# Optimization experiments

Hardware: AMD Instinct MI355X
Metric: run time of the kernel (lower is better)

The kernel has to match this reference:

```python
import jax, jax.numpy as jnp
import numpy as np

N_EMBED = 1024
N_HEAD = 16
BLOCK_SIZE = 2048
ROPE_BASE = 10000.0


def _rope_cache():
    # theta uses n_embed (full model dim) as denominator, as in the source,
    # then is truncated to head_size//2 frequencies.
    hs_half = N_EMBED // N_HEAD // 2
    j = jnp.arange(N_EMBED // 2, dtype=jnp.float32)
    theta = jnp.power(ROPE_BASE, -2.0 * j / N_EMBED)
    seq_idx = jnp.arange(BLOCK_SIZE, dtype=jnp.float32)
    idx_theta = jnp.einsum('i,j->ij', seq_idx, theta)[:, :hs_half]  # [block, hs/2]
    return jnp.stack([jnp.cos(idx_theta), jnp.sin(idx_theta)], axis=-1)  # [block, hs/2, 2]


def _apply_rope(x, cache):
    # x: [B, nh, T, hs]. FAITHFUL to source: rope indexes its cache by dim-1,
    # which here is the HEAD dim (rope is called after transpose(1,2)).
    B, d1, d2, hs = x.shape
    rc = cache[:d1, :hs // 2]            # [d1, hs/2, 2]
    rc = rc[None, :, None, :, :]          # [1, d1, 1, hs/2, 2]
    x2 = x.reshape(B, d1, d2, hs // 2, 2)
    cos, sin = rc[..., 0], rc[..., 1]
    xr, xi = x2[..., 0], x2[..., 1]
    rot = jnp.stack([xr * cos - xi * sin, xi * cos + xr * sin], axis=-1)
    return rot.reshape(B, d1, d2, hs).astype(x.dtype)


def setup_inputs() -> dict:
    key = jax.random.key(0)
    ks = jax.random.split(key, 5)
    B, T, C = 2, 2048, N_EMBED
    return {
        'x': jax.random.normal(ks[0], (B, T, C), dtype=jnp.float32),
        'w_attn': jax.random.normal(ks[1], (C, 3 * C), dtype=jnp.float32) * 0.02,
        'b_attn': jax.random.normal(ks[2], (3 * C,), dtype=jnp.float32) * 0.02,
        'w_proj': jax.random.normal(ks[3], (C, C), dtype=jnp.float32) * 0.02,
        'b_proj': jax.random.normal(ks[4], (C,), dtype=jnp.float32) * 0.02,
    }


def reference(x, w_attn, b_attn, w_proj, b_proj):
    B, T, C = x.shape
    nh, hs = N_HEAD, C // N_HEAD
    qkv = x @ w_attn + b_attn                     # [B, T, 3C]
    q, k, v = jnp.split(qkv, 3, axis=-1)
    q = q.reshape(B, T, nh, hs).transpose(0, 2, 1, 3)  # [B, nh, T, hs]
    k = k.reshape(B, T, nh, hs).transpose(0, 2, 1, 3)
    v = v.reshape(B, T, nh, hs).transpose(0, 2, 1, 3)
    cache = _rope_cache()
    q = _apply_rope(q, cache)
    k = _apply_rope(k, cache)
    scale = 1.0 / jnp.sqrt(jnp.asarray(hs, dtype=q.dtype))
    scores = jnp.einsum('bhqd,bhkd->bhqk', q, k) * scale
    causal = jnp.tril(jnp.ones((T, T), dtype=bool))
    scores = jnp.where(causal[None, None], scores, jnp.finfo(scores.dtype).min)
    attn = jax.nn.softmax(scores, axis=-1)
    y = jnp.einsum('bhqk,bhkd->bhqd', attn, v)    # [B, nh, T, hs]
    y = y.transpose(0, 2, 1, 3).reshape(B, T, C)
    return y @ w_proj + b_proj
```

## Files before the change

kernel.cpp:

```cpp
#include <hip/hip_runtime.h>
#include <hip/hip_bf16.h>
#include <math.h>

#define TSEQ 2048
#define CEMB 1024
#define NHEAD 16
#define HS 64

typedef __attribute__((ext_vector_type(8))) short bf16x8;
typedef __attribute__((ext_vector_type(4))) float f32x4;
typedef __attribute__((ext_vector_type(16))) float f32x16;
typedef unsigned int u32;

__device__ __forceinline__ void gload16(const void* g, void* l) {
    __builtin_amdgcn_global_load_lds(
        (const __attribute__((address_space(1))) unsigned int*)g,
        (__attribute__((address_space(3))) unsigned int*)l, 16, 0, 0);
}

__device__ __forceinline__ u32 pk2(float a, float b) {
    union { u32 u; __hip_bfloat16 h[2]; } t;
    t.h[0] = __float2bfloat16(a); t.h[1] = __float2bfloat16(b);
    return t.u;
}

__global__ void rope_tbl_k(float* __restrict__ tbl) {
    int i = blockIdx.x * blockDim.x + threadIdx.x;
    if (i >= NHEAD * 32) return;
    int h = i >> 5, j = i & 31;
    double theta = pow(10000.0, -2.0 * (double)j / 1024.0);
    double ang = (double)h * theta;
    tbl[2 * i + 0] = (float)cos(ang);
    tbl[2 * i + 1] = (float)sin(ang);
}

__global__ __launch_bounds__(256) void cvt_bf16_k(const float* __restrict__ in,
                                                  __hip_bfloat16* __restrict__ out) {
    int i = (blockIdx.x * 256 + threadIdx.x) * 8;
    float4 a = *(const float4*)(in + i);
    float4 b = *(const float4*)(in + i + 4);
    union { bf16x8 v; __hip_bfloat16 h[8]; } pk;
    pk.h[0] = __float2bfloat16(a.x); pk.h[1] = __float2bfloat16(a.y);
    pk.h[2] = __float2bfloat16(a.z); pk.h[3] = __float2bfloat16(a.w);
    pk.h[4] = __float2bfloat16(b.x); pk.h[5] = __float2bfloat16(b.y);
    pk.h[6] = __float2bfloat16(b.z); pk.h[7] = __float2bfloat16(b.w);
    *(bf16x8*)(out + i) = pk.v;
}

__global__ __launch_bounds__(256) void transpose_bf16_k(const float* __restrict__ src,
                                                        __hip_bfloat16* __restrict__ dst,
                                                        int K, int N) {
    __shared__ float tile[32][33];
    int n0 = blockIdx.x * 32, k0 = blockIdx.y * 32;
    int tx = threadIdx.x & 31, ty = threadIdx.x >> 5;
#pragma unroll
    for (int i = 0; i < 32; i += 8)
        tile[ty + i][tx] = src[(size_t)(k0 + ty + i) * N + n0 + tx];
    __syncthreads();
#pragma unroll
    for (int i = 0; i < 32; i += 8)
        dst[(size_t)(n0 + ty + i) * K + k0 + tx] = __float2bfloat16(tile[tx][ty + i]);
}

__global__ __launch_bounds__(256) void qkv_mfma_k(
    const __hip_bfloat16* __restrict__ Xb, const __hip_bfloat16* __restrict__ Wt,
    const float* __restrict__ bias, const float* __restrict__ tbl,
    __hip_bfloat16* __restrict__ Qb, __hip_bfloat16* __restrict__ Kb,
    __hip_bfloat16* __restrict__ Vtb)
{
    __shared__ __hip_bfloat16 Al[2][128 * 32];
    __shared__ __hip_bfloat16 Bl[2][128 * 32];
    const int tid = threadIdx.x;
    const int lane = tid & 63, w = tid >> 6;
    const int lr = lane & 15, lg = lane >> 4;
    const int wm = w >> 1, wn = w & 1;
    const int n0 = blockIdx.x * 128;
    const int m0 = blockIdx.y * 128;
    const __hip_bfloat16* gA = Xb + (size_t)(m0 + (tid >> 2)) * CEMB + (tid & 3) * 8;
    const __hip_bfloat16* gB = Wt + (size_t)(n0 + (tid >> 2)) * CEMB + (tid & 3) * 8;
#define QSTAGE(buf, kk) do { \
        gload16(gA + (kk), &Al[buf][tid * 8]); \
        gload16(gA + 64 * CEMB + (kk), &Al[buf][2048 + tid * 8]); \
        gload16(gB + (kk), &Bl[buf][tid * 8]); \
        gload16(gB + 64 * CEMB + (kk), &Bl[buf][2048 + tid * 8]); } while (0)
    f32x4 acc[4][4] = {};
    QSTAGE(0, 0);
    __syncthreads();
    for (int k0 = 0; k0 < CEMB; k0 += 32) {
        const int cur = (k0 >> 5) & 1;
        if (k0 + 32 < CEMB) QSTAGE(cur ^ 1, k0 + 32);
        bf16x8 af[4], bfr[4];
#pragma unroll
        for (int mi = 0; mi < 4; ++mi)
            af[mi] = *(const bf16x8*)&Al[cur][(wm * 64 + mi * 16 + lr) * 32 + lg * 8];
#pragma unroll
        for (int ni = 0; ni < 4; ++ni)
            bfr[ni] = *(const bf16x8*)&Bl[cur][(wn * 64 + ni * 16 + lr) * 32 + lg * 8];
#pragma unroll
        for (int mi = 0; mi < 4; ++mi)
#pragma unroll
            for (int ni = 0; ni < 4; ++ni)
                acc[mi][ni] = __builtin_amdgcn_mfma_f32_16x16x32_bf16(af[mi], bfr[ni], acc[mi][ni], 0, 0, 0);
        __syncthreads();
    }
    const int sec = (n0 >> 10);
#pragma unroll
    for (int mi = 0; mi < 4; ++mi) {
#pragma unroll
        for (int ni = 0; ni < 4; ++ni) {
            const int gcol = n0 + wn * 64 + ni * 16 + lr;
            const int c63 = gcol & 63;
            const int h = (gcol & 1023) >> 6;
            const int j = c63 >> 1;
            const float cth = tbl[(h * 32 + j) * 2 + 0];
            const float sth = tbl[(h * 32 + j) * 2 + 1];
            const float bv = bias[gcol];
            const int growb = m0 + wm * 64 + mi * 16 + lg * 4;
            const int bb = growb >> 11;
            const int t0 = growb & 2047;
            if (sec == 2) {
                union { unsigned long long u; __hip_bfloat16 hh[4]; } pk;
#pragma unroll
                for (int r = 0; r < 4; ++r) pk.hh[r] = __float2bfloat16(acc[mi][ni][r] + bv);
                *(unsigned long long*)&Vtb[(((size_t)bb * NHEAD + h) * HS + c63) * TSEQ + t0] = pk.u;
            } else {
                const float sc = (sec == 0) ? 0.18033688011112042f : 1.0f;
                __hip_bfloat16* dst = (sec == 0) ? Qb : Kb;
#pragma unroll
                for (int r = 0; r < 4; ++r) {
                    float val = acc[mi][ni][r] + bv;
                    float prt = __shfl_xor(val, 1);
                    float rot = (lr & 1) ? (val * cth + prt * sth) : (val * cth - prt * sth);
                    dst[(((size_t)bb * NHEAD + h) * TSEQ + t0 + r) * HS + c63] = __float2bfloat16(rot * sc);
                }
            }
        }
    }
#undef QSTAGE
}

__global__ __launch_bounds__(128) void attn_k(
    const __hip_bfloat16* __restrict__ Q, const __hip_bfloat16* __restrict__ K,
    const __hip_bfloat16* __restrict__ Vt, __hip_bfloat16* __restrict__ Y)
{
    __shared__ __hip_bfloat16 KsBuf[2][64 * 64];
    __shared__ __hip_bfloat16 VsBuf[2][64 * 64];
    const int tid = threadIdx.x;
    const int w = tid >> 6;
    const int lane = tid & 63;
    const int l31 = lane & 31;
    const int hi = lane >> 5;
    const int id = blockIdx.x;
    const int bh = id & 31;
    const int qb = id >> 5;
    const size_t bho = (size_t)bh * TSEQ * HS;
    const int qw = qb * 64 + w * 32;

    int srcK[4], srcV[4];
#pragma unroll
    for (int j = 0; j < 4; ++j) {
        int L = (tid + 128 * j) * 16;
        int row = L >> 7;
        int ce = ((L & 127) ^ (((row ^ (row >> 3)) & 7) << 4)) >> 1;
        srcK[j] = row * HS + ce;
        srcV[j] = row * TSEQ + ce;
    }
    const __hip_bfloat16* Kg = K + bho;
    const __hip_bfloat16* Vg = Vt + bho;
#define ASTAGE(buf, kt_) do { \
        const __hip_bfloat16* kg_ = Kg + (size_t)(kt_) * 64 * HS; \
        const __hip_bfloat16* vg_ = Vg + (size_t)(kt_) * 64; \
        char* kb_ = (char*)KsBuf[buf]; char* vb_ = (char*)VsBuf[buf]; \
        _Pragma("unroll") \
        for (int j = 0; j < 4; ++j) { \
            gload16(kg_ + srcK[j], kb_ + (tid + 128 * j) * 16); \
            gload16(vg_ + srcV[j], vb_ + (tid + 128 * j) * 16); } } while (0)

    bf16x8 qf[4];
    {
        const __hip_bfloat16* qp = Q + bho + (size_t)(qw + l31) * HS + hi * 8;
#pragma unroll
        for (int kb = 0; kb < 4; ++kb) qf[kb] = *(const bf16x8*)(qp + kb * 16);
    }
    const int base0 = l31 * 128;
    const int swz0 = ((l31 ^ (l31 >> 3)) & 7) << 4;
    const int r32 = 32 + l31;
    const int base1 = r32 * 128;
    const int swz1 = ((r32 ^ (r32 >> 3)) & 7) << 4;

    float mrow = -1e30f, lsum = 0.f;
    f32x16 o0 = {}, o1 = {};

    ASTAGE(0, 0);
    __syncthreads();
    for (int kt = 0; kt <= qb; ++kt) {
        const int cur = kt & 1;
        if (kt < qb) ASTAGE(cur ^ 1, kt + 1);
        const char* KsB = (const char*)KsBuf[cur];
        const char* VsB = (const char*)VsBuf[cur];
        const bool do1 = (w == 1) || (kt < qb);
        f32x16 s0 = {}, s1 = {};
#pragma unroll
        for (int kb = 0; kb < 4; ++kb) {
            bf16x8 kf = *(const bf16x8*)(KsB + base0 + ((kb * 32 + hi * 16) ^ swz0));
            s0 = __builtin_amdgcn_mfma_f32_32x32x16_bf16(kf, qf[kb], s0, 0, 0, 0);
        }
        if (do1) {
#pragma unroll
            for (int kb = 0; kb < 4; ++kb) {
                bf16x8 kf = *(const bf16x8*)(KsB + base1 + ((kb * 32 + hi * 16) ^ swz1));
                s1 = __builtin_amdgcn_mfma_f32_32x32x16_bf16(kf, qf[kb], s1, 0, 0, 0);
            }
        }
        if (kt == qb) {
            if (w == 0) {
#pragma unroll
                for (int r = 0; r < 16; ++r) {
                    int crow = (r & 3) + 8 * (r >> 2) + 4 * hi;
                    if (crow > l31) s0[r] = -1e30f;
                }
            } else {
#pragma unroll
                for (int r = 0; r < 16; ++r) {
                    int crow = (r & 3) + 8 * (r >> 2) + 4 * hi;
                    if (crow > l31) s1[r] = -1e30f;
                }
            }
        }
        float mx = s0[0];
#pragma unroll
        for (int r = 1; r < 16; ++r) mx = fmaxf(mx, s0[r]);
        if (do1) {
#pragma unroll
            for (int r = 0; r < 16; ++r) mx = fmaxf(mx, s1[r]);
        }
        mx = fmaxf(mx, __shfl_xor(mx, 32));
        const float mn = fmaxf(mrow, mx);
        const float alpha = __builtin_amdgcn_exp2f(mrow - mn);
        mrow = mn;
        float ls = 0.f;
#pragma unroll
        for (int r = 0; r < 16; ++r) { s0[r] = __builtin_amdgcn_exp2f(s0[r] - mn); ls += s0[r]; }
        if (do1) {
#pragma unroll
            for (int r = 0; r < 16; ++r) { s1[r] = __builtin_amdgcn_exp2f(s1[r] - mn); ls += s1[r]; }
        }
        ls += __shfl_xor(ls, 32);
        lsum = lsum * alpha + ls;
        o0 = o0 * alpha;
        o1 = o1 * alpha;
        union { u32 u[4]; bf16x8 v; } pa[4];
        {
            u32 w01 = pk2(s0[0], s0[1]),   w23 = pk2(s0[2], s0[3]);
            u32 w45 = pk2(s0[4], s0[5]),   w67 = pk2(s0[6], s0[7]);
            u32 w89 = pk2(s0[8], s0[9]),   wab = pk2(s0[10], s0[11]);
            u32 wcd = pk2(s0[12], s0[13]), wef = pk2(s0[14], s0[15]);
            u32 xa = __shfl_xor(hi ? w01 : w45, 32);
            u32 xb = __shfl_xor(hi ? w23 : w67, 32);
            u32 xc = __shfl_xor(hi ? w89 : wcd, 32);
            u32 xd = __shfl_xor(hi ? wab : wef, 32);
            if (hi == 0) {
                pa[0].u[0] = w01; pa[0].u[1] = w23; pa[0].u[2] = xa;  pa[0].u[3] = xb;
                pa[1].u[0] = w89; pa[1].u[1] = wab; pa[1].u[2] = xc;  pa[1].u[3] = xd;
            } else {
                pa[0].u[0] = xa;  pa[0].u[1] = xb;  pa[0].u[2] = w45; pa[0].u[3] = w67;
                pa[1].u[0] = xc;  pa[1].u[1] = xd;  pa[1].u[2] = wcd; pa[1].u[3] = wef;
            }
        }
        if (do1) {
            u32 w01 = pk2(s1[0], s1[1]),   w23 = pk2(s1[2], s1[3]);
            u32 w45 = pk2(s1[4], s1[5]),   w67 = pk2(s1[6], s1[7]);
            u32 w89 = pk2(s1[8], s1[9]),   wab = pk2(s1[10], s1[11]);
            u32 wcd = pk2(s1[12], s1[13]), wef = pk2(s1[14], s1[15]);
            u32 xa = __shfl_xor(hi ? w01 : w45, 32);
            u32 xb = __shfl_xor(hi ? w23 : w67, 32);
            u32 xc = __shfl_xor(hi ? w89 : wcd, 32);
            u32 xd = __shfl_xor(hi ? wab : wef, 32);
            if (hi == 0) {
                pa[2].u[0] = w01; pa[2].u[1] = w23; pa[2].u[2] = xa;  pa[2].u[3] = xb;
                pa[3].u[0] = w89; pa[3].u[1] = wab; pa[3].u[2] = xc;  pa[3].u[3] = xd;
            } else {
                pa[2].u[0] = xa;  pa[2].u[1] = xb;  pa[2].u[2] = w45; pa[2].u[3] = w67;
                pa[3].u[0] = xc;  pa[3].u[1] = xd;  pa[3].u[2] = wcd; pa[3].u[3] = wef;
            }
        }
#pragma unroll
        for (int ks = 0; ks < 2; ++ks) {
            bf16x8 vf0 = *(const bf16x8*)(VsB + base0 + ((ks * 32 + hi * 16) ^ swz0));
            o0 = __builtin_amdgcn_mfma_f32_32x32x16_bf16(vf0, pa[ks].v, o0, 0, 0, 0);
            bf16x8 vf1 = *(const bf16x8*)(VsB + base1 + ((ks * 32 + hi * 16) ^ swz1));
            o1 = __builtin_amdgcn_mfma_f32_32x32x16_bf16(vf1, pa[ks].v, o1, 0, 0, 0);
        }
        if (do1) {
#pragma unroll
            for (int ks = 2; ks < 4; ++ks) {
                bf16x8 vf0 = *(const bf16x8*)(VsB + base0 + ((ks * 32 + hi * 16) ^ swz0));
                o0 = __builtin_amdgcn_mfma_f32_32x32x16_bf16(vf0, pa[ks].v, o0, 0, 0, 0);
                bf16x8 vf1 = *(const bf16x8*)(VsB + base1 + ((ks * 32 + hi * 16) ^ swz1));
                o1 = __builtin_amdgcn_mfma_f32_32x32x16_bf16(vf1, pa[ks].v, o1, 0, 0, 0);
            }
        }
        __syncthreads();
    }
    __syncthreads();
    {
        char* T = (char*)KsBuf[0] + w * 4096;
        const float inv = 1.f / lsum;
        const int tsw = (l31 & 7) << 4;
#pragma unroll
        for (int r = 0; r < 16; ++r) {
            int d0 = (r & 3) + 8 * (r >> 2) + 4 * hi;
            *(__hip_bfloat16*)(T + base0 + ((d0 * 2) ^ tsw)) = __float2bfloat16(o0[r] * inv);
            *(__hip_bfloat16*)(T + base0 + (((d0 + 32) * 2) ^ tsw)) = __float2bfloat16(o1[r] * inv);
        }
        const int b = bh >> 4, h = bh & 15;
#pragma unroll
        for (int p = 0; p < 4; ++p) {
            int q = p * 8 + (lane >> 3);
            int colb = ((lane & 7) * 16) ^ ((q & 7) << 4);
            bf16x8 v = *(const bf16x8*)(T + q * 128 + colb);
            *(bf16x8*)(Y + ((size_t)b * TSEQ + qw + q) * CEMB + h * HS + (lane & 7) * 8) = v;
        }
    }
#undef ASTAGE
}

__global__ __launch_bounds__(256) void proj_mfma_k(
    const __hip_bfloat16* __restrict__ Ab, const __hip_bfloat16* __restrict__ Wt,
    const float* __restrict__ bias, float* __restrict__ out)
{
    __shared__ __hip_bfloat16 Al[2][128 * 32];
    __shared__ __hip_bfloat16 Bl[2][128 * 32];
    const int tid = threadIdx.x;
    const int lane = tid & 63, w = tid >> 6;
    const int lr = lane & 15, lg = lane >> 4;
    const int wm = w >> 1, wn = w & 1;
    const int n0 = blockIdx.x * 128;
    const int m0 = blockIdx.y * 128;
    const __hip_bfloat16* gA = Ab + (size_t)(m0 + (tid >> 2)) * CEMB + (tid & 3) * 8;
    const __hip_bfloat16* gB = Wt + (size_t)(n0 + (tid >> 2)) * CEMB + (tid & 3) * 8;
#define PSTAGE(buf, kk) do { \
        gload16(gA + (kk), &Al[buf][tid * 8]); \
        gload16(gA + 64 * CEMB + (kk), &Al[buf][2048 + tid * 8]); \
        gload16(gB + (kk), &Bl[buf][tid * 8]); \
        gload16(gB + 64 * CEMB + (kk), &Bl[buf][2048 + tid * 8]); } while (0)
    f32x4 acc[4][4] = {};
    PSTAGE(0, 0);
    __syncthreads();
    for (int k0 = 0; k0 < CEMB; k0 += 32) {
        const int cur = (k0 >> 5) & 1;
        if (k0 + 32 < CEMB) PSTAGE(cur ^ 1, k0 + 32);
        bf16x8 af[4], bfr[4];
#pragma unroll
        for (int mi = 0; mi < 4; ++mi)
            af[mi] = *(const bf16x8*)&Al[cur][(wm * 64 + mi * 16 + lr) * 32 + lg * 8];
#pragma unroll
        for (int ni = 0; ni < 4; ++ni)
            bfr[ni] = *(const bf16x8*)&Bl[cur][(wn * 64 + ni * 16 + lr) * 32 + lg * 8];
#pragma unroll
        for (int mi = 0; mi < 4; ++mi)
#pragma unroll
            for (int ni = 0; ni < 4; ++ni)
                acc[mi][ni] = __builtin_amdgcn_mfma_f32_16x16x32_bf16(af[mi], bfr[ni], acc[mi][ni], 0, 0, 0);
        __syncthreads();
    }
#pragma unroll
    for (int mi = 0; mi < 4; ++mi) {
#pragma unroll
        for (int ni = 0; ni < 4; ++ni) {
            const int gcol = n0 + wn * 64 + ni * 16 + lr;
            const float bv = bias[gcol];
            const int growb = m0 + wm * 64 + mi * 16 + lg * 4;
#pragma unroll
            for (int r = 0; r < 4; ++r)
                out[(size_t)(growb + r) * CEMB + gcol] = acc[mi][ni][r] + bv;
        }
    }
#undef PSTAGE
}

extern "C" void kernel_launch(void* const* d_in, const int* in_sizes, int n_in,
                              void* d_out, int out_size, void* d_ws, size_t ws_size,
                              hipStream_t stream)
{
    const float* x      = (const float*)d_in[0];
    const float* w_attn = (const float*)d_in[1];
    const float* b_attn = (const float*)d_in[2];
    const float* w_proj = (const float*)d_in[3];
    const float* b_proj = (const float*)d_in[4];
    float* out = (float*)d_out;
    char* base = (char*)d_ws;

    const size_t MB = 1048576;
    float* tbl          = (float*)base;
    __hip_bfloat16* Xb  = (__hip_bfloat16*)(base + 4096);
    __hip_bfloat16* Wta = (__hip_bfloat16*)(base + 4096 + 8 * MB);
    __hip_bfloat16* Wpt = (__hip_bfloat16*)(base + 4096 + 14 * MB);
    __hip_bfloat16* Qb  = (__hip_bfloat16*)(base + 4096 + 16 * MB);
    __hip_bfloat16* Kb  = (__hip_bfloat16*)(base + 4096 + 24 * MB);
    __hip_bfloat16* Vtb = (__hip_bfloat16*)(base + 4096 + 32 * MB);
    __hip_bfloat16* Yb  = Xb;

    rope_tbl_k<<<1, 512, 0, stream>>>(tbl);
    cvt_bf16_k<<<2048, 256, 0, stream>>>(x, Xb);
    transpose_bf16_k<<<dim3(96, 32), 256, 0, stream>>>(w_attn, Wta, CEMB, 3 * CEMB);
    transpose_bf16_k<<<dim3(32, 32), 256, 0, stream>>>(w_proj, Wpt, CEMB, CEMB);
    qkv_mfma_k<<<dim3(24, 32), 256, 0, stream>>>(Xb, Wta, b_attn, tbl, Qb, Kb, Vtb);
    attn_k<<<1024, 128, 0, stream>>>(Qb, Kb, Vtb, Yb);
    proj_mfma_k<<<dim3(8, 32), 256, 0, stream>>>(Yb, Wpt, b_proj, out);
}
```

Measured before the change: 149.7 us.

## Stage V-transpose stores through LDS, serpentine q-block order, MFMA priority hints

The QKV GEMM epilogue for the V section now writes the tile into a swizzled LDS buffer, then each thread emits 16-byte contiguous stores to the transposed V layout instead of scattered 8-byte stores. The attention kernel remaps block IDs so q-blocks are visited in a serpentine order within groups of eight, which spreads causal work more evenly across concurrently running blocks. It also raises wave priority around the MFMA sections with s_setprio. Costs are an extra LDS round trip and barrier in the V epilogue, plus scheduling behaviour that may depend on occupancy.

```diff
diff --git a/kernel.cpp b/kernel.cpp
--- a/kernel.cpp
+++ b/kernel.cpp
@@ -11,6 +11,7 @@
 typedef __attribute__((ext_vector_type(4))) float f32x4;
 typedef __attribute__((ext_vector_type(16))) float f32x16;
 typedef unsigned int u32;
+typedef unsigned long long u64;
 
 __device__ __forceinline__ void gload16(const void* g, void* l) {
     __builtin_amdgcn_global_load_lds(
@@ -68,8 +69,7 @@
     __hip_bfloat16* __restrict__ Qb, __hip_bfloat16* __restrict__ Kb,
     __hip_bfloat16* __restrict__ Vtb)
 {
-    __shared__ __hip_bfloat16 Al[2][128 * 32];
-    __shared__ __hip_bfloat16 Bl[2][128 * 32];
+    __shared__ __hip_bfloat16 SM[4][128 * 32];
     const int tid = threadIdx.x;
     const int lane = tid & 63, w = tid >> 6;
     const int lr = lane & 15, lg = lane >> 4;
@@ -79,10 +79,10 @@
     const __hip_bfloat16* gA = Xb + (size_t)(m0 + (tid >> 2)) * CEMB + (tid & 3) * 8;
     const __hip_bfloat16* gB = Wt + (size_t)(n0 + (tid >> 2)) * CEMB + (tid & 3) * 8;
 #define QSTAGE(buf, kk) do { \
-        gload16(gA + (kk), &Al[buf][tid * 8]); \
-        gload16(gA + 64 * CEMB + (kk), &Al[buf][2048 + tid * 8]); \
-        gload16(gB + (kk), &Bl[buf][tid * 8]); \
-        gload16(gB + 64 * CEMB + (kk), &Bl[buf][2048 + tid * 8]); } while (0)
+        gload16(gA + (kk), &SM[buf][tid * 8]); \
+        gload16(gA + 64 * CEMB + (kk), &SM[buf][2048 + tid * 8]); \
+        gload16(gB + (kk), &SM[2 + (buf)][tid * 8]); \
+        gload16(gB + 64 * CEMB + (kk), &SM[2 + (buf)][2048 + tid * 8]); } while (0)
     f32x4 acc[4][4] = {};
     QSTAGE(0, 0);
     __syncthreads();
@@ -92,10 +92,10 @@
         bf16x8 af[4], bfr[4];
 #pragma unroll
         for (int mi = 0; mi < 4; ++mi)
-            af[mi] = *(const bf16x8*)&Al[cur][(wm * 64 + mi * 16 + lr) * 32 + lg * 8];
+            af[mi] = *(const bf16x8*)&SM[cur][(wm * 64 + mi * 16 + lr) * 32 + lg * 8];
 #pragma unroll
         for (int ni = 0; ni < 4; ++ni)
-            bfr[ni] = *(const bf16x8*)&Bl[cur][(wn * 64 + ni * 16 + lr) * 32 + lg * 8];
+            bfr[ni] = *(const bf16x8*)&SM[2 + cur][(wn * 64 + ni * 16 + lr) * 32 + lg * 8];
 #pragma unroll
         for (int mi = 0; mi < 4; ++mi)
 #pragma unroll
@@ -104,26 +104,46 @@
         __syncthreads();
     }
     const int sec = (n0 >> 10);
-#pragma unroll
-    for (int mi = 0; mi < 4; ++mi) {
-#pragma unroll
-        for (int ni = 0; ni < 4; ++ni) {
-            const int gcol = n0 + wn * 64 + ni * 16 + lr;
-            const int c63 = gcol & 63;
-            const int h = (gcol & 1023) >> 6;
-            const int j = c63 >> 1;
-            const float cth = tbl[(h * 32 + j) * 2 + 0];
-            const float sth = tbl[(h * 32 + j) * 2 + 1];
-            const float bv = bias[gcol];
-            const int growb = m0 + wm * 64 + mi * 16 + lg * 4;
-            const int bb = growb >> 11;
-            const int t0 = growb & 2047;
-            if (sec == 2) {
-                union { unsigned long long u; __hip_bfloat16 hh[4]; } pk;
+    const int bb = m0 >> 11;
+    const int t0v = m0 & 2047;
+    if (sec == 2) {
+        char* T = (char*)SM;
+#pragma unroll
+        for (int mi = 0; mi < 4; ++mi) {
+#pragma unroll
+            for (int ni = 0; ni < 4; ++ni) {
+                const int nl = wn * 64 + ni * 16 + lr;
+                const float bv = bias[n0 + nl];
+                const int mb = wm * 64 + mi * 16 + lg * 4;
+                union { u64 u; __hip_bfloat16 hh[4]; } pk;
 #pragma unroll
                 for (int r = 0; r < 4; ++r) pk.hh[r] = __float2bfloat16(acc[mi][ni][r] + bv);
-                *(unsigned long long*)&Vtb[(((size_t)bb * NHEAD + h) * HS + c63) * TSEQ + t0] = pk.u;
-            } else {
+                *(u64*)(T + nl * 256 + ((mb * 2) ^ ((nl & 7) << 4))) = pk.u;
+            }
+        }
+        __syncthreads();
+        const int h0 = (n0 & 1023) >> 6;
+#pragma unroll
+        for (int i = 0; i < 8; ++i) {
+            int cid = tid + 256 * i;
+            int n = cid >> 4, mc = cid & 15;
+            bf16x8 v = *(const bf16x8*)(T + n * 256 + ((mc * 16) ^ ((n & 7) << 4)));
+            *(bf16x8*)&Vtb[(((size_t)bb * NHEAD + h0 + (n >> 6)) * HS + (n & 63)) * TSEQ + t0v + mc * 8] = v;
+        }
+    } else {
+#pragma unroll
+        for (int mi = 0; mi < 4; ++mi) {
+#pragma unroll
+            for (int ni = 0; ni < 4; ++ni) {
+                const int gcol = n0 + wn * 64 + ni * 16 + lr;
+                const int c63 = gcol & 63;
+                const int h = (gcol & 1023) >> 6;
+                const int j = c63 >> 1;
+                const float cth = tbl[(h * 32 + j) * 2 + 0];
+                const float sth = tbl[(h * 32 + j) * 2 + 1];
+                const float bv = bias[gcol];
+                const int growb = m0 + wm * 64 + mi * 16 + lg * 4;
+                const int t0 = growb & 2047;
                 const float sc = (sec == 0) ? 0.18033688011112042f : 1.0f;
                 __hip_bfloat16* dst = (sec == 0) ? Qb : Kb;
 #pragma unroll
@@ -152,7 +172,8 @@
     const int hi = lane >> 5;
     const int id = blockIdx.x;
     const int bh = id & 31;
-    const int qb = id >> 5;
+    const int g = id >> 5, ga = g & 7, gb = g >> 3;
+    const int qb = gb * 8 + ((gb & 1) ? (7 - ga) : ga);
     const size_t bho = (size_t)bh * TSEQ * HS;
     const int qw = qb * 64 + w * 32;
 
@@ -200,6 +221,7 @@
         const char* VsB = (const char*)VsBuf[cur];
         const bool do1 = (w == 1) || (kt < qb);
         f32x16 s0 = {}, s1 = {};
+        __builtin_amdgcn_s_setprio(1);
 #pragma unroll
         for (int kb = 0; kb < 4; ++kb) {
             bf16x8 kf = *(const bf16x8*)(KsB + base0 + ((kb * 32 + hi * 16) ^ swz0));
@@ -212,6 +234,7 @@
                 s1 = __builtin_amdgcn_mfma_f32_32x32x16_bf16(kf, qf[kb], s1, 0, 0, 0);
             }
         }
+        __builtin_amdgcn_s_setprio(0);
         if (kt == qb) {
             if (w == 0) {
 #pragma unroll
@@ -284,6 +307,7 @@
                 pa[3].u[0] = xc;  pa[3].u[1] = xd;  pa[3].u[2] = wcd; pa[3].u[3] = wef;
             }
         }
+        __builtin_amdgcn_s_setprio(1);
 #pragma unroll
         for (int ks = 0; ks < 2; ++ks) {
             bf16x8 vf0 = *(const bf16x8*)(VsB + base0 + ((ks * 32 + hi * 16) ^ swz0));
@@ -300,6 +324,7 @@
                 o1 = __builtin_amdgcn_mfma_f32_32x32x16_bf16(vf1, pa[ks].v, o1, 0, 0, 0);
             }
         }
+        __builtin_amdgcn_s_setprio(0);
         __syncthreads();
     }
     __syncthreads();
```

Measured after the change: 147.6 us. No clear change (-1.4%).
